# Kernel tuning notes

Hardware: AMD Instinct MI355X
Metric: run time of the kernel (lower is better)

The kernel has to match this reference:

```python
import jax, jax.numpy as jnp
import numpy as np

N_NODES = 100000


def _gcn_edges(edge_index, num_nodes):
    # Add self-loops and compute symmetric GCN normalization per edge.
    src = jnp.concatenate([edge_index[0], jnp.arange(num_nodes, dtype=edge_index.dtype)])
    dst = jnp.concatenate([edge_index[1], jnp.arange(num_nodes, dtype=edge_index.dtype)])
    deg = jnp.zeros((num_nodes,), jnp.float32).at[dst].add(1.0)
    dinv = jnp.where(deg > 0, jax.lax.rsqrt(deg), 0.0)
    norm = dinv[src] * dinv[dst]  # [E+N]
    return src, dst, norm


def _gcn_conv(x, W, b, src, dst, norm, num_nodes):
    h = x @ W                         # [N, d_out] transform first (d_out <= d_in)
    msg = h[src] * norm[:, None]      # [E, d_out] gather + scale
    agg = jax.ops.segment_sum(msg, dst, num_segments=num_nodes)
    return agg + b


def setup_inputs() -> dict:
    key = jax.random.key(0)
    k = jax.random.split(key, 8)
    n, e, d_in, d_out = N_NODES, 1600000, 128, 64
    hid = 2 * d_out
    s = lambda fan: 1.0 / np.sqrt(fan)
    return {
        "x": jax.random.normal(k[0], (n, d_in), jnp.float32),
        "edge_index": jax.random.randint(k[1], (2, e), 0, n, jnp.int64),
        "W1": jax.random.normal(k[2], (d_in, hid), jnp.float32) * s(d_in),
        "b1": jnp.zeros((hid,), jnp.float32),
        "Wmu": jax.random.normal(k[3], (hid, d_out), jnp.float32) * s(hid),
        "bmu": jnp.zeros((d_out,), jnp.float32),
        "Wls": jax.random.normal(k[4], (hid, d_out), jnp.float32) * s(hid),
        "bls": jnp.zeros((d_out,), jnp.float32),
    }


def reference(x, edge_index, W1, b1, Wmu, bmu, Wls, bls):
    n = x.shape[0]
    src, dst, norm = _gcn_edges(edge_index, n)
    h = jax.nn.relu(_gcn_conv(x, W1, b1, src, dst, norm, n))
    mu = _gcn_conv(h, Wmu, bmu, src, dst, norm, n)
    logstd = _gcn_conv(h, Wls, bls, src, dst, norm, n)
    return mu, logstd
```

## Files before the change

kernel.cpp:

```cpp
#include <hip/hip_runtime.h>

#define DIN 128
#define HID 128
#define DOUT 64
#define NCHUNK 196
#define BSH 9
#define NB1MAX 256
#define BSLACK 1540

typedef unsigned short ushort_t;
typedef unsigned int uint_t;
typedef __attribute__((ext_vector_type(4))) short s4v;
typedef __attribute__((ext_vector_type(4))) float f4v;

#if defined(__has_builtin)
#if __has_builtin(__builtin_amdgcn_mfma_f32_16x16x16bf16_1k)
#define MFMA16(a, b, c) __builtin_amdgcn_mfma_f32_16x16x16bf16_1k(a, b, c, 0, 0, 0)
#endif
#endif
#ifndef MFMA16
static __device__ inline f4v mfma16_asm(s4v a, s4v b, f4v c) {
  asm volatile("v_mfma_f32_16x16x16_bf16 %0, %1, %2, %0" : "+v"(c) : "v"(a), "v"(b));
  return c;
}
#define MFMA16(a, b, c) mfma16_asm(a, b, c)
#endif

static inline int ceil_div(int a, int b) { return (a + b - 1) / b; }

__device__ inline ushort_t f2bf(float f) {
  uint_t u = __float_as_uint(f);
  u += 0x7fff + ((u >> 16) & 1);
  return (ushort_t)(u >> 16);
}
__device__ inline uint_t pack2bf(float a, float b) {
  return (uint_t)f2bf(a) | ((uint_t)f2bf(b) << 16);
}
__device__ inline float2 bf2x2(uint_t u) {
  return make_float2(__uint_as_float(u << 16), __uint_as_float(u & 0xffff0000u));
}

__device__ inline int blk_scan_incl(int v, int* ws) {
  int t = threadIdx.x, lane = t & 63, w = t >> 6;
#pragma unroll
  for (int d = 1; d < 64; d <<= 1) {
    int u = __shfl_up(v, d, 64);
    if (lane >= d) v += u;
  }
  if (lane == 63) ws[w] = v;
  __syncthreads();
  if (w == 0) {
    int s = (lane < 4) ? ws[lane] : 0;
#pragma unroll
    for (int d = 1; d < 4; d <<= 1) {
      int u = __shfl_up(s, d, 64);
      if (lane >= d) s += u;
    }
    if (lane < 4) ws[lane] = s;
  }
  __syncthreads();
  if (w > 0) v += ws[w - 1];
  return v;
}


__global__ __launch_bounds__(256) void k_bhist(const int* __restrict__ dst, int E, int CH,
                                               int nb1, int* __restrict__ counts) {
  __shared__ uint_t cnt[NB1MAX];
  int t = threadIdx.x, c = blockIdx.x;
  for (int i = t; i < nb1; i += 256) cnt[i] = 0;
  __syncthreads();
  int e0 = c * CH, e1 = min(E, e0 + CH);
  for (int i = e0 + t; i < e1; i += 256) atomicAdd(&cnt[((uint_t)dst[i]) >> BSH], 1u);
  __syncthreads();
  for (int i = t; i < nb1; i += 256) counts[c * nb1 + i] = (int)cnt[i];
}

__global__ __launch_bounds__(256) void k_bscan(const int* __restrict__ counts, int nb1,
                                               int* __restrict__ chunk_off,
                                               int* __restrict__ btot) {
  __shared__ int ws[4];
  int b = blockIdx.x, t = threadIdx.x;
  int v = (t < NCHUNK) ? counts[t * nb1 + b] : 0;
  int incl = blk_scan_incl(v, ws);
  if (t < NCHUNK) chunk_off[t * nb1 + b] = incl - v;
  if (t == NCHUNK - 1) btot[b] = incl;
}

__global__ __launch_bounds__(256) void k_bbase(const int* __restrict__ btot, int nb1, int E,
                                               int* __restrict__ bbase) {
  __shared__ int ws[4];
  int t = threadIdx.x;
  int v = (t < nb1) ? btot[t] : 0;
  int incl = blk_scan_incl(v, ws);
  if (t < nb1) bbase[t] = incl - v;
  if (t == 0) bbase[nb1] = E;
}

__global__ __launch_bounds__(256) void k_bscatter(const int* __restrict__ src,
                                                  const int* __restrict__ dst, int E, int CH,
                                                  int nb1, const int* __restrict__ bbase,
                                                  const int* __restrict__ chunk_off,
                                                  uint_t* __restrict__ tmp) {
  __shared__ uint_t cur[NB1MAX];
  int t = threadIdx.x, c = blockIdx.x;
  for (int i = t; i < nb1; i += 256)
    cur[i] = (uint_t)(bbase[i] + chunk_off[c * nb1 + i]);
  __syncthreads();
  int e0 = c * CH, e1 = min(E, e0 + CH);
  for (int i = e0 + t; i < e1; i += 256) {
    uint_t d = (uint_t)dst[i];
    uint_t s = (uint_t)src[i];
    uint_t p = atomicAdd(&cur[d >> BSH], 1u);
    tmp[p] = ((d & ((1u << BSH) - 1)) << 17) | s;
  }
}

__global__ __launch_bounds__(256) void k_bfinal(const uint_t* __restrict__ tmp,
                                                const int* __restrict__ bbase, int N, int nb1,
                                                uint_t* __restrict__ csr,
                                                int* __restrict__ row_ptr,
                                                int* __restrict__ row_end,
                                                float* __restrict__ dinv) {
  __shared__ uint_t cnt[1 << BSH];
  __shared__ uint_t ppfx[1 << BSH];
  __shared__ uint_t cur[1 << BSH];
  int b = blockIdx.x, t = threadIdx.x;
  int seg0 = bbase[b], seg1 = bbase[b + 1];
  int pb = ((seg0 + 3) & ~3) + BSLACK * b;
  for (int i = t; i < (1 << BSH); i += 256) cnt[i] = 0;
  __syncthreads();
  for (int i = seg0 + t; i < seg1; i += 256) atomicAdd(&cnt[tmp[i] >> 17], 1u);
  __syncthreads();
  if (t < 64) {
    uint_t pc[8];
    uint_t s = 0;
#pragma unroll
    for (int k = 0; k < 8; k++) {
      pc[k] = (cnt[t * 8 + k] + 3u) & ~3u;
      s += pc[k];
    }
    int incl = (int)s;
#pragma unroll
    for (int d = 1; d < 64; d <<= 1) {
      int u = __shfl_up(incl, d, 64);
      if (t >= d) incl += u;
    }
    uint_t excl = (uint_t)incl - s;
#pragma unroll
    for (int k = 0; k < 8; k++) {
      ppfx[t * 8 + k] = excl;
      excl += pc[k];
    }
  }
  __syncthreads();
  int nd0 = b << BSH;
  for (int i = t; i < (1 << BSH); i += 256) {
    cur[i] = ppfx[i];
    int g = nd0 + i;
    if (g < N) {
      row_ptr[g] = pb + (int)ppfx[i];
      row_end[g] = pb + (int)(ppfx[i] + ((cnt[i] + 3u) & ~3u));
      dinv[g] = rsqrtf((float)cnt[i] + 1.0f);
    }
  }
  __syncthreads();
  for (int i = seg0 + t; i < seg1; i += 256) {
    uint_t v = tmp[i];
    uint_t pos = atomicAdd(&cur[v >> 17], 1u);
    csr[pb + (int)pos] = v & 0x1FFFFu;
  }
  __syncthreads();
  for (int i = t; i < (1 << BSH); i += 256) {
    uint_t e0 = cur[i];
    uint_t e1 = ppfx[i] + ((cnt[i] + 3u) & ~3u);
    for (uint_t k = e0; k < e1; k++) csr[pb + (int)k] = (uint_t)N;
  }
}


__global__ __launch_bounds__(256) void k_prep(const float* __restrict__ W1,
                                              const float* __restrict__ Wmu,
                                              const float* __restrict__ Wls,
                                              ushort_t* __restrict__ Wt1,
                                              ushort_t* __restrict__ Wt2) {
  int idx = blockIdx.x * 256 + threadIdx.x;
  int j = idx >> 7, k = idx & 127;
  Wt1[j * 128 + k] = f2bf(W1[k * 128 + j]);
  Wt2[j * 128 + k] = f2bf(j < 64 ? Wmu[k * 64 + j] : Wls[k * 64 + (j - 64)]);
}


__global__ __launch_bounds__(256) void k_gemm1(const float* __restrict__ A,
                                               const ushort_t* __restrict__ Wt,
                                               ushort_t* __restrict__ C, int n) {
  __shared__ ushort_t Ws[128][132];
  int t = threadIdx.x;
#pragma unroll
  for (int i = 0; i < 16; i++) {
    int f = t + 256 * i;
    int rowj = f >> 5, seg = f & 31;
    *(uint2*)&Ws[rowj][seg * 4] = *(const uint2*)(Wt + rowj * 128 + seg * 4);
  }
  __syncthreads();
  int w = t >> 6, lane = t & 63;
  int rl = lane & 15, g = lane >> 4;
  int row = blockIdx.x * 64 + w * 16 + rl;
  bool valid = row < n;
  const float* Ar = A + (size_t)row * DIN + 4 * g;
  s4v af[8];
#pragma unroll
  for (int kk = 0; kk < 8; kk++) {
    float4 v = make_float4(0.f, 0.f, 0.f, 0.f);
    if (valid) v = *(const float4*)(Ar + kk * 16);
    s4v a;
    a[0] = (short)f2bf(v.x);
    a[1] = (short)f2bf(v.y);
    a[2] = (short)f2bf(v.z);
    a[3] = (short)f2bf(v.w);
    af[kk] = a;
  }
  f4v acc[8];
#pragma unroll
  for (int ct = 0; ct < 8; ct++) acc[ct] = (f4v)0.f;
#pragma unroll
  for (int kk = 0; kk < 8; kk++) {
    int ko = kk * 16 + 4 * g;
#pragma unroll
    for (int ct = 0; ct < 8; ct++) {
      s4v b = *(s4v*)&Ws[ct * 16 + rl][ko];
      acc[ct] = MFMA16(af[kk], b, acc[ct]);
    }
  }
  int gr0 = blockIdx.x * 64 + w * 16 + 4 * g;
#pragma unroll
  for (int i = 0; i < 4; i++) {
    int gr = gr0 + i;
    if (gr < n) {
#pragma unroll
      for (int ct = 0; ct < 8; ct++)
        C[(size_t)gr * HID + ct * 16 + rl] = f2bf(acc[ct][i]);
    }
  }
}


__global__ __launch_bounds__(256) void k_agg(const ushort_t* __restrict__ H,
                                             const int* __restrict__ row_ptr,
                                             const int* __restrict__ row_end,
                                             const uint_t* __restrict__ csr,
                                             const float* __restrict__ dinv,
                                             const float* __restrict__ bias,
                                             ushort_t* __restrict__ out, int n, int relu) {
  int node = (blockIdx.x * blockDim.x + threadIdx.x) >> 6;
  int lane = threadIdx.x & 63;
  if (node >= n) return;
  const char* Hb = (const char*)H;
  const char* Db = (const char*)dinv;
  uint_t loff = (uint_t)lane << 2;
  float dn = dinv[node];
  int j = row_ptr[node], end = row_end[node];
  float2 hs = bf2x2(*(const uint_t*)(Hb + ((size_t)(((uint_t)node << 8) | loff))));
  float ax = dn * hs.x, ay = dn * hs.y;
  if (j < end) {
    uint4 c = *(const uint4*)(csr + j);
    while (true) {
      int jn = j + 4;
      bool more = jn < end;
      uint4 cn;
      if (more) cn = *(const uint4*)(csr + jn);
      float w0 = *(const float*)(Db + (size_t)(c.x << 2));
      float w1 = *(const float*)(Db + (size_t)(c.y << 2));
      float w2 = *(const float*)(Db + (size_t)(c.z << 2));
      float w3 = *(const float*)(Db + (size_t)(c.w << 2));
      uint_t v0 = *(const uint_t*)(Hb + (size_t)((c.x << 8) | loff));
      uint_t v1 = *(const uint_t*)(Hb + (size_t)((c.y << 8) | loff));
      uint_t v2 = *(const uint_t*)(Hb + (size_t)((c.z << 8) | loff));
      uint_t v3 = *(const uint_t*)(Hb + (size_t)((c.w << 8) | loff));
      float2 f0 = bf2x2(v0), f1 = bf2x2(v1), f2 = bf2x2(v2), f3 = bf2x2(v3);
      ax += w0 * f0.x; ay += w0 * f0.y;
      ax += w1 * f1.x; ay += w1 * f1.y;
      ax += w2 * f2.x; ay += w2 * f2.y;
      ax += w3 * f3.x; ay += w3 * f3.y;
      if (!more) break;
      c = cn;
      j = jn;
    }
  }
  ax *= dn;
  ay *= dn;
  if (bias) {
    ax += bias[2 * lane];
    ay += bias[2 * lane + 1];
  }
  if (relu) {
    ax = fmaxf(ax, 0.f);
    ay = fmaxf(ay, 0.f);
  }
  ((uint_t*)out)[(size_t)node * 64 + lane] = pack2bf(ax, ay);
}


__global__ __launch_bounds__(256) void k_gemm2(const ushort_t* __restrict__ A,
                                               const ushort_t* __restrict__ Wt,
                                               const float* __restrict__ bmu,
                                               const float* __restrict__ bls,
                                               float* __restrict__ out, int n) {
  __shared__ ushort_t Ws[128][132];
  int t = threadIdx.x;
#pragma unroll
  for (int i = 0; i < 16; i++) {
    int f = t + 256 * i;
    int rowj = f >> 5, seg = f & 31;
    *(uint2*)&Ws[rowj][seg * 4] = *(const uint2*)(Wt + rowj * 128 + seg * 4);
  }
  __syncthreads();
  int w = t >> 6, lane = t & 63;
  int rl = lane & 15, g = lane >> 4;
  int row = blockIdx.x * 64 + w * 16 + rl;
  bool valid = row < n;
  const ushort_t* Ar = A + (size_t)row * HID + 4 * g;
  s4v af[8];
#pragma unroll
  for (int kk = 0; kk < 8; kk++) {
    s4v a = (s4v)0;
    if (valid) a = *(const s4v*)(Ar + kk * 16);
    af[kk] = a;
  }
  f4v acc[8];
#pragma unroll
  for (int ct = 0; ct < 8; ct++) acc[ct] = (f4v)0.f;
#pragma unroll
  for (int kk = 0; kk < 8; kk++) {
    int ko = kk * 16 + 4 * g;
#pragma unroll
    for (int ct = 0; ct < 8; ct++) {
      s4v b = *(s4v*)&Ws[ct * 16 + rl][ko];
      acc[ct] = MFMA16(af[kk], b, acc[ct]);
    }
  }
  int gr0 = blockIdx.x * 64 + w * 16 + 4 * g;
#pragma unroll
  for (int ct = 0; ct < 8; ct++) {
    int col = ct * 16 + rl;
    float bv;
    size_t obase;
    int cc;
    if (ct < 4) {
      bv = bmu[col];
      obase = 0;
      cc = col;
    } else {
      bv = bls[col - 64];
      obase = (size_t)n * DOUT;
      cc = col - 64;
    }
#pragma unroll
    for (int i = 0; i < 4; i++) {
      int gr = gr0 + i;
      if (gr < n) out[obase + (size_t)gr * DOUT + cc] = acc[ct][i] + bv;
    }
  }
}


extern "C" void kernel_launch(void* const* d_in, const int* in_sizes, int n_in,
                              void* d_out, int out_size, void* d_ws, size_t ws_size,
                              hipStream_t stream) {
  const float* x   = (const float*)d_in[0];
  const int*   ei  = (const int*)d_in[1];
  const float* W1  = (const float*)d_in[2];
  const float* b1  = (const float*)d_in[3];
  const float* Wmu = (const float*)d_in[4];
  const float* bmu = (const float*)d_in[5];
  const float* Wls = (const float*)d_in[6];
  const float* bls = (const float*)d_in[7];
  float* out = (float*)d_out;

  const int N = in_sizes[0] / DIN;
  const int E = in_sizes[1] / 2;
  const int* esrc = ei;
  const int* edst = ei + E;
  const int nb1 = ceil_div(N, 1 << BSH);
  const int CH = ceil_div(E, NCHUNK);

  char* ws = (char*)d_ws;
  size_t off = 0;
  auto alloc = [&](size_t bytes) -> void* {
    void* p = ws + off;
    off = (off + bytes + 255) & ~(size_t)255;
    return p;
  };
  ushort_t* xWb   = (ushort_t*)alloc((size_t)(N + 1) * HID * sizeof(ushort_t));
  ushort_t* h     = (ushort_t*)alloc((size_t)(N + 1) * HID * sizeof(ushort_t));
  uint_t* csr     = (uint_t*)alloc(((size_t)E + (size_t)(BSLACK + 8) * nb1 + 16) * 4);
  uint_t* tmp     = (uint_t*)alloc((size_t)E * 4);
  int* counts     = (int*)alloc((size_t)NCHUNK * nb1 * 4);
  int* chunk_off  = (int*)alloc((size_t)NCHUNK * nb1 * 4);
  int* btot       = (int*)alloc((size_t)nb1 * 4);
  int* bbase      = (int*)alloc((size_t)(nb1 + 1) * 4);
  int* row_ptr    = (int*)alloc((size_t)N * 4);
  int* row_end    = (int*)alloc((size_t)N * 4);
  float* dinv     = (float*)alloc((size_t)(N + 1) * 4);
  ushort_t* wt1b  = (ushort_t*)alloc((size_t)HID * HID * 2);
  ushort_t* wt2b  = (ushort_t*)alloc((size_t)HID * HID * 2);
  (void)ws_size; (void)n_in; (void)out_size;

  hipMemsetAsync((char*)xWb + (size_t)N * 256, 0, 256, stream);
  hipMemsetAsync((char*)h + (size_t)N * 256, 0, 256, stream);
  hipMemsetAsync(dinv + N, 0, 4, stream);

  k_prep<<<64, 256, 0, stream>>>(W1, Wmu, Wls, wt1b, wt2b);

  k_bhist<<<NCHUNK, 256, 0, stream>>>(edst, E, CH, nb1, counts);
  k_bscan<<<nb1, 256, 0, stream>>>(counts, nb1, chunk_off, btot);
  k_bbase<<<1, 256, 0, stream>>>(btot, nb1, E, bbase);
  k_bscatter<<<NCHUNK, 256, 0, stream>>>(esrc, edst, E, CH, nb1, bbase, chunk_off, tmp);
  k_bfinal<<<nb1, 256, 0, stream>>>(tmp, bbase, N, nb1, csr, row_ptr, row_end, dinv);

  k_gemm1<<<ceil_div(N, 64), 256, 0, stream>>>(x, wt1b, xWb, N);
  k_agg<<<ceil_div(N, 4), 256, 0, stream>>>(xWb, row_ptr, row_end, csr, dinv, b1, h, N, 1);

  k_agg<<<ceil_div(N, 4), 256, 0, stream>>>(h, row_ptr, row_end, csr, dinv, nullptr, xWb, N, 0);
  k_gemm2<<<ceil_div(N, 64), 256, 0, stream>>>(xWb, wt2b, bmu, bls, out, N);
}
```

Before: 239.0 us.

## Prescale features by dinv, fuse setup kernels, and widen histogram chunking

Applies the symmetric normalization by prescaling source rows by dinv, in the GEMM1 epilogue and in the first aggregation's output. This removes the per-edge dinv gather in both aggregation passes. It also merges the weight prep, histogram and memsets into one setup kernel, and folds the bucket-base scan into the scatter and final kernels so k_bbase is gone. Chunk count rises to 784 for more parallelism in the histogram and scatter. The cost is redundant scans in every block, a larger counts array, and extra bf16 rounding because the prescaled values are stored in bf16.

Measured after the change: 216.5 us. 1.1x faster.

```diff
diff --git a/kernel.cpp b/kernel.cpp
--- a/kernel.cpp
+++ b/kernel.cpp
@@ -3,7 +3,7 @@
 #define DIN 128
 #define HID 128
 #define DOUT 64
-#define NCHUNK 196
+#define NCHUNK 784
 #define BSH 9
 #define NB1MAX 256
 #define BSLACK 1540
@@ -40,7 +40,7 @@
   return make_float2(__uint_as_float(u << 16), __uint_as_float(u & 0xffff0000u));
 }
 
-__device__ inline int blk_scan_incl(int v, int* ws) {
+__device__ inline int blk_scan_incl(int v, int* ws, int nw) {
   int t = threadIdx.x, lane = t & 63, w = t >> 6;
 #pragma unroll
   for (int d = 1; d < 64; d <<= 1) {
@@ -50,13 +50,12 @@
   if (lane == 63) ws[w] = v;
   __syncthreads();
   if (w == 0) {
-    int s = (lane < 4) ? ws[lane] : 0;
-#pragma unroll
-    for (int d = 1; d < 4; d <<= 1) {
+    int s = (lane < nw) ? ws[lane] : 0;
+    for (int d = 1; d < nw; d <<= 1) {
       int u = __shfl_up(s, d, 64);
       if (lane >= d) s += u;
     }
-    if (lane < 4) ws[lane] = s;
+    if (lane < nw) ws[lane] = s;
   }
   __syncthreads();
   if (w > 0) v += ws[w - 1];
@@ -64,48 +63,70 @@
 }
 
 
-__global__ __launch_bounds__(256) void k_bhist(const int* __restrict__ dst, int E, int CH,
-                                               int nb1, int* __restrict__ counts) {
+__global__ __launch_bounds__(512) void k_setup(const int* __restrict__ dst, int E, int CH,
+                                               int nb1, int* __restrict__ counts,
+                                               const float* __restrict__ W1,
+                                               const float* __restrict__ Wmu,
+                                               const float* __restrict__ Wls,
+                                               ushort_t* __restrict__ Wt1,
+                                               ushort_t* __restrict__ Wt2,
+                                               ushort_t* __restrict__ xWb,
+                                               ushort_t* __restrict__ h,
+                                               float* __restrict__ dinv, int N) {
   __shared__ uint_t cnt[NB1MAX];
-  int t = threadIdx.x, c = blockIdx.x;
-  for (int i = t; i < nb1; i += 256) cnt[i] = 0;
-  __syncthreads();
-  int e0 = c * CH, e1 = min(E, e0 + CH);
-  for (int i = e0 + t; i < e1; i += 256) atomicAdd(&cnt[((uint_t)dst[i]) >> BSH], 1u);
-  __syncthreads();
-  for (int i = t; i < nb1; i += 256) counts[c * nb1 + i] = (int)cnt[i];
+  int b = blockIdx.x, t = threadIdx.x;
+  if (b < NCHUNK) {
+    for (int i = t; i < nb1; i += 512) cnt[i] = 0;
+    __syncthreads();
+    int e0 = b * CH, e1 = min(E, e0 + CH);
+    for (int i = e0 + t; i < e1; i += 512) atomicAdd(&cnt[((uint_t)dst[i]) >> BSH], 1u);
+    __syncthreads();
+    for (int i = t; i < nb1; i += 512) counts[b * nb1 + i] = (int)cnt[i];
+  } else if (b < NCHUNK + 32) {
+    int idx = (b - NCHUNK) * 512 + t;
+    int j = idx >> 7, k = idx & 127;
+    Wt1[j * 128 + k] = f2bf(W1[k * 128 + j]);
+    Wt2[j * 128 + k] = f2bf(j < 64 ? Wmu[k * 64 + j] : Wls[k * 64 + (j - 64)]);
+  } else {
+    if (t < 64) ((uint_t*)(xWb + (size_t)N * HID))[t] = 0;
+    else if (t < 128) ((uint_t*)(h + (size_t)N * HID))[t - 64] = 0;
+    else if (t == 128) dinv[N] = 0.f;
+  }
 }
 
 __global__ __launch_bounds__(256) void k_bscan(const int* __restrict__ counts, int nb1,
                                                int* __restrict__ chunk_off,
                                                int* __restrict__ btot) {
-  __shared__ int ws[4];
+  __shared__ int ws[8];
+  __shared__ int shc;
   int b = blockIdx.x, t = threadIdx.x;
-  int v = (t < NCHUNK) ? counts[t * nb1 + b] : 0;
-  int incl = blk_scan_incl(v, ws);
-  if (t < NCHUNK) chunk_off[t * nb1 + b] = incl - v;
-  if (t == NCHUNK - 1) btot[b] = incl;
-}
-
-__global__ __launch_bounds__(256) void k_bbase(const int* __restrict__ btot, int nb1, int E,
-                                               int* __restrict__ bbase) {
-  __shared__ int ws[4];
-  int t = threadIdx.x;
-  int v = (t < nb1) ? btot[t] : 0;
-  int incl = blk_scan_incl(v, ws);
-  if (t < nb1) bbase[t] = incl - v;
-  if (t == 0) bbase[nb1] = E;
+  int carry = 0;
+#pragma unroll
+  for (int r = 0; r < NCHUNK / 256 + 1; r++) {
+    int idx = r * 256 + t;
+    int v = (idx < NCHUNK) ? counts[idx * nb1 + b] : 0;
+    int incl = blk_scan_incl(v, ws, 4) + carry;
+    if (idx < NCHUNK) chunk_off[idx * nb1 + b] = incl - v;
+    if (t == 255) shc = incl;
+    __syncthreads();
+    carry = shc;
+  }
+  if (t == 0) btot[b] = carry;
 }
 
 __global__ __launch_bounds__(256) void k_bscatter(const int* __restrict__ src,
                                                   const int* __restrict__ dst, int E, int CH,
-                                                  int nb1, const int* __restrict__ bbase,
+                                                  int nb1, const int* __restrict__ btot,
                                                   const int* __restrict__ chunk_off,
                                                   uint_t* __restrict__ tmp) {
+  __shared__ int ws[8];
   __shared__ uint_t cur[NB1MAX];
   int t = threadIdx.x, c = blockIdx.x;
-  for (int i = t; i < nb1; i += 256)
-    cur[i] = (uint_t)(bbase[i] + chunk_off[c * nb1 + i]);
+  {
+    int v = (t < nb1) ? btot[t] : 0;
+    int incl = blk_scan_incl(v, ws, 4);
+    if (t < nb1) cur[t] = (uint_t)(incl - v + chunk_off[c * nb1 + t]);
+  }
   __syncthreads();
   int e0 = c * CH, e1 = min(E, e0 + CH);
   for (int i = e0 + t; i < e1; i += 256) {
@@ -116,21 +137,31 @@
   }
 }
 
-__global__ __launch_bounds__(256) void k_bfinal(const uint_t* __restrict__ tmp,
-                                                const int* __restrict__ bbase, int N, int nb1,
+__global__ __launch_bounds__(512) void k_bfinal(const uint_t* __restrict__ tmp,
+                                                const int* __restrict__ btot, int N, int nb1,
                                                 uint_t* __restrict__ csr,
                                                 int* __restrict__ row_ptr,
                                                 int* __restrict__ row_end,
                                                 float* __restrict__ dinv) {
+  __shared__ int ws[8];
+  __shared__ int sseg0, sseg1;
   __shared__ uint_t cnt[1 << BSH];
   __shared__ uint_t ppfx[1 << BSH];
   __shared__ uint_t cur[1 << BSH];
   int b = blockIdx.x, t = threadIdx.x;
-  int seg0 = bbase[b], seg1 = bbase[b + 1];
+  {
+    int v = (t < nb1) ? btot[t] : 0;
+    int incl = blk_scan_incl(v, ws, 8);
+    if (t == b) {
+      sseg0 = incl - v;
+      sseg1 = incl;
+    }
+  }
+  for (int i = t; i < (1 << BSH); i += 512) cnt[i] = 0;
+  __syncthreads();
+  int seg0 = sseg0, seg1 = sseg1;
   int pb = ((seg0 + 3) & ~3) + BSLACK * b;
-  for (int i = t; i < (1 << BSH); i += 256) cnt[i] = 0;
-  __syncthreads();
-  for (int i = seg0 + t; i < seg1; i += 256) atomicAdd(&cnt[tmp[i] >> 17], 1u);
+  for (int i = seg0 + t; i < seg1; i += 512) atomicAdd(&cnt[tmp[i] >> 17], 1u);
   __syncthreads();
   if (t < 64) {
     uint_t pc[8];
@@ -155,7 +186,7 @@
   }
   __syncthreads();
   int nd0 = b << BSH;
-  for (int i = t; i < (1 << BSH); i += 256) {
+  for (int i = t; i < (1 << BSH); i += 512) {
     cur[i] = ppfx[i];
     int g = nd0 + i;
     if (g < N) {
@@ -165,13 +196,13 @@
     }
   }
   __syncthreads();
-  for (int i = seg0 + t; i < seg1; i += 256) {
+  for (int i = seg0 + t; i < seg1; i += 512) {
     uint_t v = tmp[i];
     uint_t pos = atomicAdd(&cur[v >> 17], 1u);
     csr[pb + (int)pos] = v & 0x1FFFFu;
   }
   __syncthreads();
-  for (int i = t; i < (1 << BSH); i += 256) {
+  for (int i = t; i < (1 << BSH); i += 512) {
     uint_t e0 = cur[i];
     uint_t e1 = ppfx[i] + ((cnt[i] + 3u) & ~3u);
     for (uint_t k = e0; k < e1; k++) csr[pb + (int)k] = (uint_t)N;
@@ -179,20 +210,9 @@
 }
 
 
-__global__ __launch_bounds__(256) void k_prep(const float* __restrict__ W1,
-                                              const float* __restrict__ Wmu,
-                                              const float* __restrict__ Wls,
-                                              ushort_t* __restrict__ Wt1,
-                                              ushort_t* __restrict__ Wt2) {
-  int idx = blockIdx.x * 256 + threadIdx.x;
-  int j = idx >> 7, k = idx & 127;
-  Wt1[j * 128 + k] = f2bf(W1[k * 128 + j]);
-  Wt2[j * 128 + k] = f2bf(j < 64 ? Wmu[k * 64 + j] : Wls[k * 64 + (j - 64)]);
-}
-
-
 __global__ __launch_bounds__(256) void k_gemm1(const float* __restrict__ A,
                                                const ushort_t* __restrict__ Wt,
+                                               const float* __restrict__ dinv,
                                                ushort_t* __restrict__ C, int n) {
   __shared__ ushort_t Ws[128][132];
   int t = threadIdx.x;
@@ -237,9 +257,10 @@
   for (int i = 0; i < 4; i++) {
     int gr = gr0 + i;
     if (gr < n) {
+      float dv = dinv[gr];
 #pragma unroll
       for (int ct = 0; ct < 8; ct++)
-        C[(size_t)gr * HID + ct * 16 + rl] = f2bf(acc[ct][i]);
+        C[(size_t)gr * HID + ct * 16 + rl] = f2bf(dv * acc[ct][i]);
     }
   }
 }
@@ -251,17 +272,17 @@
                                              const uint_t* __restrict__ csr,
                                              const float* __restrict__ dinv,
                                              const float* __restrict__ bias,
-                                             ushort_t* __restrict__ out, int n, int relu) {
+                                             ushort_t* __restrict__ out, int n,
+                                             int prescale_relu) {
   int node = (blockIdx.x * blockDim.x + threadIdx.x) >> 6;
   int lane = threadIdx.x & 63;
   if (node >= n) return;
   const char* Hb = (const char*)H;
-  const char* Db = (const char*)dinv;
   uint_t loff = (uint_t)lane << 2;
   float dn = dinv[node];
   int j = row_ptr[node], end = row_end[node];
   float2 hs = bf2x2(*(const uint_t*)(Hb + ((size_t)(((uint_t)node << 8) | loff))));
-  float ax = dn * hs.x, ay = dn * hs.y;
+  float ax = hs.x, ay = hs.y;
   if (j < end) {
     uint4 c = *(const uint4*)(csr + j);
     while (true) {
@@ -269,19 +290,15 @@
       bool more = jn < end;
       uint4 cn;
       if (more) cn = *(const uint4*)(csr + jn);
-      float w0 = *(const float*)(Db + (size_t)(c.x << 2));
-      float w1 = *(const float*)(Db + (size_t)(c.y << 2));
-      float w2 = *(const float*)(Db + (size_t)(c.z << 2));
-      float w3 = *(const float*)(Db + (size_t)(c.w << 2));
       uint_t v0 = *(const uint_t*)(Hb + (size_t)((c.x << 8) | loff));
       uint_t v1 = *(const uint_t*)(Hb + (size_t)((c.y << 8) | loff));
       uint_t v2 = *(const uint_t*)(Hb + (size_t)((c.z << 8) | loff));
       uint_t v3 = *(const uint_t*)(Hb + (size_t)((c.w << 8) | loff));
       float2 f0 = bf2x2(v0), f1 = bf2x2(v1), f2 = bf2x2(v2), f3 = bf2x2(v3);
-      ax += w0 * f0.x; ay += w0 * f0.y;
-      ax += w1 * f1.x; ay += w1 * f1.y;
-      ax += w2 * f2.x; ay += w2 * f2.y;
-      ax += w3 * f3.x; ay += w3 * f3.y;
+      ax += f0.x + f1.x;
+      ay += f0.y + f1.y;
+      ax += f2.x + f3.x;
+      ay += f2.y + f3.y;
       if (!more) break;
       c = cn;
       j = jn;
@@ -289,13 +306,9 @@
   }
   ax *= dn;
   ay *= dn;
-  if (bias) {
-    ax += bias[2 * lane];
-    ay += bias[2 * lane + 1];
-  }
-  if (relu) {
-    ax = fmaxf(ax, 0.f);
-    ay = fmaxf(ay, 0.f);
+  if (prescale_relu) {
+    ax = fmaxf(ax + bias[2 * lane], 0.f) * dn;
+    ay = fmaxf(ay + bias[2 * lane + 1], 0.f) * dn;
   }
   ((uint_t*)out)[(size_t)node * 64 + lane] = pack2bf(ax, ay);
 }
@@ -398,7 +411,6 @@
   int* counts     = (int*)alloc((size_t)NCHUNK * nb1 * 4);
   int* chunk_off  = (int*)alloc((size_t)NCHUNK * nb1 * 4);
   int* btot       = (int*)alloc((size_t)nb1 * 4);
-  int* bbase      = (int*)alloc((size_t)(nb1 + 1) * 4);
   int* row_ptr    = (int*)alloc((size_t)N * 4);
   int* row_end    = (int*)alloc((size_t)N * 4);
   float* dinv     = (float*)alloc((size_t)(N + 1) * 4);
@@ -406,19 +418,13 @@
   ushort_t* wt2b  = (ushort_t*)alloc((size_t)HID * HID * 2);
   (void)ws_size; (void)n_in; (void)out_size;
 
-  hipMemsetAsync((char*)xWb + (size_t)N * 256, 0, 256, stream);
-  hipMemsetAsync((char*)h + (size_t)N * 256, 0, 256, stream);
-  hipMemsetAsync(dinv + N, 0, 4, stream);
-
-  k_prep<<<64, 256, 0, stream>>>(W1, Wmu, Wls, wt1b, wt2b);
-
-  k_bhist<<<NCHUNK, 256, 0, stream>>>(edst, E, CH, nb1, counts);
+  k_setup<<<NCHUNK + 33, 512, 0, stream>>>(edst, E, CH, nb1, counts, W1, Wmu, Wls, wt1b, wt2b,
+                                           xWb, h, dinv, N);
   k_bscan<<<nb1, 256, 0, stream>>>(counts, nb1, chunk_off, btot);
-  k_bbase<<<1, 256, 0, stream>>>(btot, nb1, E, bbase);
-  k_bscatter<<<NCHUNK, 256, 0, stream>>>(esrc, edst, E, CH, nb1, bbase, chunk_off, tmp);
-  k_bfinal<<<nb1, 256, 0, stream>>>(tmp, bbase, N, nb1, csr, row_ptr, row_end, dinv);
-
-  k_gemm1<<<ceil_div(N, 64), 256, 0, stream>>>(x, wt1b, xWb, N);
+  k_bscatter<<<NCHUNK, 256, 0, stream>>>(esrc, edst, E, CH, nb1, btot, chunk_off, tmp);
+  k_bfinal<<<nb1, 512, 0, stream>>>(tmp, btot, N, nb1, csr, row_ptr, row_end, dinv);
+
+  k_gemm1<<<ceil_div(N, 64), 256, 0, stream>>>(x, wt1b, dinv, xWb, N);
   k_agg<<<ceil_div(N, 4), 256, 0, stream>>>(xWb, row_ptr, row_end, csr, dinv, b1, h, N, 1);
 
   k_agg<<<ceil_div(N, 4), 256, 0, stream>>>(h, row_ptr, row_end, csr, dinv, nullptr, xWb, N, 0);
```
